# Kernel tuning notes

Hardware: AMD Instinct MI355X
Metric: run time of the kernel (lower is better)

Reference implementation:

```python
import jax, jax.numpy as jnp
import numpy as np

N_NODES = 50000
N_EDGES = 800000
NDIM_IN = 64
EDIM = 64
HID = 152  # size_embedding
NDIM_OUT = 64


def _linear(x, W, b):
    # torch nn.Linear: y = x @ W.T + b
    return jnp.matmul(x, W.T) + b


def _sage_layer(nf, ef, Wm, bm, Wa, ba, src, dst):
    # message: gather src node feats, concat edge feats, linear -> [E,1,F]
    m = _linear(jnp.concatenate([nf[src], ef], axis=2), Wm, bm)
    # mean scatter-reduce to dst nodes (zero for nodes with no in-edges)
    s = jax.ops.segment_sum(m, dst, num_segments=N_NODES)
    deg = jax.ops.segment_sum(jnp.ones((m.shape[0],), m.dtype), dst, num_segments=N_NODES)
    h_neigh = s / jnp.maximum(deg, 1.0)[:, None, None]
    # update: concat self + neighbor agg, linear, relu
    return jax.nn.relu(_linear(jnp.concatenate([nf, h_neigh], axis=2), Wa, ba))


def setup_inputs() -> dict:
    key = jax.random.key(0)
    ks = jax.random.split(key, 16)
    def lin_params(kw, kb, fan_in, fan_out):
        bound = 1.0 / np.sqrt(fan_in)
        W = jax.random.uniform(kw, (fan_out, fan_in), jnp.float32, -bound, bound)
        b = jax.random.uniform(kb, (fan_out,), jnp.float32, -bound, bound)
        return W, b
    nfeats = jax.random.normal(ks[0], (N_NODES, 1, NDIM_IN), jnp.float32)
    efeats = jax.random.normal(ks[1], (N_EDGES, 1, EDIM), jnp.float32)
    src = jax.random.randint(ks[2], (N_EDGES,), 0, N_NODES, jnp.int32)
    dst = jax.random.randint(ks[3], (N_EDGES,), 0, N_NODES, jnp.int32)
    Wm1, bm1 = lin_params(ks[4], ks[5], NDIM_IN + EDIM, HID)
    Wa1, ba1 = lin_params(ks[6], ks[7], NDIM_IN + HID, HID)
    Wm2, bm2 = lin_params(ks[8], ks[9], HID + EDIM, HID)
    Wa2, ba2 = lin_params(ks[10], ks[11], HID + HID, HID)
    Wm3, bm3 = lin_params(ks[12], ks[13], HID + EDIM, NDIM_OUT)
    Wa3, ba3 = lin_params(ks[14], ks[15], HID + NDIM_OUT, NDIM_OUT)
    return {
        "nfeats": nfeats, "efeats": efeats,
        "Wm1": Wm1, "bm1": bm1, "Wa1": Wa1, "ba1": ba1,
        "Wm2": Wm2, "bm2": bm2, "Wa2": Wa2, "ba2": ba2,
        "Wm3": Wm3, "bm3": bm3, "Wa3": Wa3, "ba3": ba3,
        "src": src, "dst": dst,
    }


def reference(nfeats, efeats, Wm1, bm1, Wa1, ba1, Wm2, bm2, Wa2, ba2,
              Wm3, bm3, Wa3, ba3, src, dst):
    # dropout is identity in eval mode
    h = _sage_layer(nfeats, efeats, Wm1, bm1, Wa1, ba1, src, dst)
    h = _sage_layer(h, efeats, Wm2, bm2, Wa2, ba2, src, dst)
    h = _sage_layer(h, efeats, Wm3, bm3, Wa3, ba3, src, dst)
    return h.sum(axis=1)  # [N, ndim_out]
```

## Files before the change

### kernel.cpp

```cpp
#include <hip/hip_runtime.h>


#define NN 50000
#define NE 800000
#define NIN 64
#define EDIM_ 64
#define HID_ 152
#define NOUT 64
#define PADN 50176

__global__ __launch_bounds__(256) void hist_kernel(const int* __restrict__ dst,
                                                   int* __restrict__ ideg) {
    int e = blockIdx.x * 256 + threadIdx.x;
    if (e < NE) atomicAdd(&ideg[dst[e]], 1);
}

__global__ __launch_bounds__(256) void scan1_kernel(const int* __restrict__ in,
                                                    int* __restrict__ out,
                                                    int* __restrict__ bsum) {
    __shared__ int ws[4];
    int t = threadIdx.x;
    int base = blockIdx.x * 1024 + t * 4;
    int a0 = in[base], a1 = in[base + 1], a2 = in[base + 2], a3 = in[base + 3];
    int s = a0 + a1 + a2 + a3;
    int lane = t & 63, wid = t >> 6;
    int v = s;
#pragma unroll
    for (int d = 1; d < 64; d <<= 1) {
        int u = __shfl_up(v, d);
        if (lane >= d) v += u;
    }
    if (lane == 63) ws[wid] = v;
    __syncthreads();
    int wofs = 0;
    if (wid > 0) wofs += ws[0];
    if (wid > 1) wofs += ws[1];
    if (wid > 2) wofs += ws[2];
    int excl = wofs + v - s;
    out[base] = excl;
    out[base + 1] = excl + a0;
    out[base + 2] = excl + a0 + a1;
    out[base + 3] = excl + a0 + a1 + a2;
    if (t == 255) bsum[blockIdx.x] = wofs + v;
}

__global__ __launch_bounds__(64) void scan2_kernel(int* __restrict__ bsum, int nb) {
    int t = threadIdx.x;
    int orig = (t < nb) ? bsum[t] : 0;
    int v = orig;
#pragma unroll
    for (int d = 1; d < 64; d <<= 1) {
        int u = __shfl_up(v, d);
        if (t >= d) v += u;
    }
    if (t < nb) bsum[t] = v - orig;
}

__global__ __launch_bounds__(256) void scan3_kernel(int* __restrict__ out,
                                                    const int* __restrict__ bsum) {
    int base = blockIdx.x * 1024 + threadIdx.x * 4;
    int b = bsum[blockIdx.x];
    out[base] += b; out[base + 1] += b; out[base + 2] += b; out[base + 3] += b;
}

__global__ __launch_bounds__(256) void scatter_edges_kernel(const int* __restrict__ src,
                                                            const int* __restrict__ dst,
                                                            int* __restrict__ cursor,
                                                            int* __restrict__ csr_nf,
                                                            int* __restrict__ csr_ef) {
    int e = blockIdx.x * 256 + threadIdx.x;
    if (e >= NE) return;
    int d = dst[e];
    int pos = atomicAdd(&cursor[d], 1);
    csr_nf[pos] = src[e];
    csr_ef[pos] = e;
}

template <int F>
__global__ __launch_bounds__(256) void agg_kernel(const float* __restrict__ table,
                                                  const int* __restrict__ rows,
                                                  const int* __restrict__ off,
                                                  float* __restrict__ out) {
    constexpr int C = F / 4;
    constexpr int NPW = 64 / C;
    int t = threadIdx.x;
    int lane = t & 63, wid = t >> 6;
    int sub = lane / C;
    int ch = lane - sub * C;
    int n = (blockIdx.x * 4 + wid) * NPW + sub;
    if (sub >= NPW || n >= NN) return;
    int s = off[n], e = off[n + 1];
    float ax0 = 0.f, ax1 = 0.f, ax2 = 0.f, ax3 = 0.f;
    float bx0 = 0.f, bx1 = 0.f, bx2 = 0.f, bx3 = 0.f;
    int i = s;
    for (; i + 1 < e; i += 2) {
        int r0 = rows[i], r1 = rows[i + 1];
        float4 v0 = *(const float4*)(table + (size_t)r0 * F + ch * 4);
        float4 v1 = *(const float4*)(table + (size_t)r1 * F + ch * 4);
        ax0 += v0.x; ax1 += v0.y; ax2 += v0.z; ax3 += v0.w;
        bx0 += v1.x; bx1 += v1.y; bx2 += v1.z; bx3 += v1.w;
    }
    if (i < e) {
        int r0 = rows[i];
        float4 v0 = *(const float4*)(table + (size_t)r0 * F + ch * 4);
        ax0 += v0.x; ax1 += v0.y; ax2 += v0.z; ax3 += v0.w;
    }
    float4 r;
    r.x = ax0 + bx0; r.y = ax1 + bx1; r.z = ax2 + bx2; r.w = ax3 + bx3;
    *(float4*)(out + (size_t)n * F + ch * 4) = r;
}

template <int K1, int K2, int NT, bool MSG>
__global__ __launch_bounds__(256) void gemm_kernel(const float* __restrict__ X1,
                                                   const float* __restrict__ X2,
                                                   const float* __restrict__ W,
                                                   const float* __restrict__ bias,
                                                   const int* __restrict__ off,
                                                   float* __restrict__ out) {
    constexpr int KT = K1 + K2;
    constexpr int NKS = (KT + 15) / 16;
    __shared__ float Xs[16][132];
    __shared__ float Ws[16][68];

    const int t = threadIdx.x;
    const int m0 = blockIdx.x * 128;
    const int n0 = blockIdx.y * 64;

    const int xm = t >> 1;
    const int xh = (t & 1) * 8;
    const int wn = t >> 2;
    const int wc = (t & 3) * 4;

    const int tx = t & 15;
    const int ty = t >> 4;

    const int xrow = m0 + xm;
    const bool xok = xrow < NN;
    const bool wok = (n0 + wn) < NT;
    const float* __restrict__ xrp1 = X1 + (size_t)xrow * K1;
    const float* __restrict__ xrp2 = X2 + (size_t)xrow * K2;
    const float* __restrict__ wrp  = W + (size_t)(n0 + wn) * KT;

    float acc[8][4] = {};
    float4 rx0, rx1, rw;

    auto loadT = [&](int k0) {
        const int kv = k0 + xh;
        rx0 = make_float4(0.f, 0.f, 0.f, 0.f);
        rx1 = rx0;
        if (xok && kv < KT) {
            const float* p = (kv < K1) ? (xrp1 + kv) : (xrp2 + (kv - K1));
            rx0 = *(const float4*)p;
            rx1 = *(const float4*)(p + 4);
        }
        rw = make_float4(0.f, 0.f, 0.f, 0.f);
        const int kw = k0 + wc;
        if (wok && kw < KT) rw = *(const float4*)(wrp + kw);
    };
    auto storeT = [&]() {
        Xs[xh + 0][xm] = rx0.x; Xs[xh + 1][xm] = rx0.y;
        Xs[xh + 2][xm] = rx0.z; Xs[xh + 3][xm] = rx0.w;
        Xs[xh + 4][xm] = rx1.x; Xs[xh + 5][xm] = rx1.y;
        Xs[xh + 6][xm] = rx1.z; Xs[xh + 7][xm] = rx1.w;
        Ws[wc + 0][wn] = rw.x;  Ws[wc + 1][wn] = rw.y;
        Ws[wc + 2][wn] = rw.z;  Ws[wc + 3][wn] = rw.w;
    };

    loadT(0);
    storeT();
    __syncthreads();

    for (int s = 0; s < NKS; ++s) {
        const bool more = (s + 1 < NKS);
        if (more) loadT((s + 1) * 16);
#pragma unroll
        for (int k = 0; k < 16; ++k) {
            const float4 xa = *(const float4*)&Xs[k][ty * 8];
            const float4 xb = *(const float4*)&Xs[k][ty * 8 + 4];
            const float4 wv = *(const float4*)&Ws[k][tx * 4];
            const float xv[8] = {xa.x, xa.y, xa.z, xa.w, xb.x, xb.y, xb.z, xb.w};
#pragma unroll
            for (int i = 0; i < 8; ++i) {
                acc[i][0] += xv[i] * wv.x;
                acc[i][1] += xv[i] * wv.y;
                acc[i][2] += xv[i] * wv.z;
                acc[i][3] += xv[i] * wv.w;
            }
        }
        if (more) {
            __syncthreads();
            storeT();
            __syncthreads();
        }
    }

    const int o0 = n0 + tx * 4;
    if (o0 >= NT) return;
    const float4 bv = *(const float4*)(bias + o0);
#pragma unroll
    for (int i = 0; i < 8; ++i) {
        const int n = m0 + ty * 8 + i;
        if (n >= NN) break;
        float4 r;
        if (MSG) {
            float d = (float)(off[n + 1] - off[n]);
            float inv = 1.0f / fmaxf(d, 1.0f);
            r.x = (acc[i][0] + d * bv.x) * inv;
            r.y = (acc[i][1] + d * bv.y) * inv;
            r.z = (acc[i][2] + d * bv.z) * inv;
            r.w = (acc[i][3] + d * bv.w) * inv;
        } else {
            r.x = fmaxf(acc[i][0] + bv.x, 0.0f);
            r.y = fmaxf(acc[i][1] + bv.y, 0.0f);
            r.z = fmaxf(acc[i][2] + bv.z, 0.0f);
            r.w = fmaxf(acc[i][3] + bv.w, 0.0f);
        }
        *(float4*)(out + (size_t)n * NT + o0) = r;
    }
}

extern "C" void kernel_launch(void* const* d_in, const int* in_sizes, int n_in,
                              void* d_out, int out_size, void* d_ws, size_t ws_size,
                              hipStream_t stream) {
    const float* nfeats = (const float*)d_in[0];
    const float* efeats = (const float*)d_in[1];
    const float* Wm1 = (const float*)d_in[2];
    const float* bm1 = (const float*)d_in[3];
    const float* Wa1 = (const float*)d_in[4];
    const float* ba1 = (const float*)d_in[5];
    const float* Wm2 = (const float*)d_in[6];
    const float* bm2 = (const float*)d_in[7];
    const float* Wa2 = (const float*)d_in[8];
    const float* ba2 = (const float*)d_in[9];
    const float* Wm3 = (const float*)d_in[10];
    const float* bm3 = (const float*)d_in[11];
    const float* Wa3 = (const float*)d_in[12];
    const float* ba3 = (const float*)d_in[13];
    const int* src = (const int*)d_in[14];
    const int* dst = (const int*)d_in[15];
    float* out = (float*)d_out;

    int* iws = (int*)d_ws;
    int* ideg   = iws;
    int* off    = iws + PADN;
    int* cursor = iws + 2 * PADN;
    int* csr_nf = iws + 3 * PADN;
    int* csr_ef = csr_nf + NE;
    float* B = (float*)(csr_ef + NE);
    float* P = B + 3200000;
    float* Q = P + 7600000;
    float* R = Q + 7600000;

    const int BLK = 256;
    auto cdiv = [](long long a, long long b) { return (int)((a + b - 1) / b); };
    dim3 g152(cdiv(NN, 128), cdiv(152, 64));
    dim3 g64(cdiv(NN, 128), 1);
    const int NB = PADN / 1024;

    hipMemsetAsync(ideg, 0, (size_t)PADN * 4, stream);
    hist_kernel<<<cdiv(NE, BLK), BLK, 0, stream>>>(dst, ideg);
    scan1_kernel<<<NB, 256, 0, stream>>>(ideg, off, cursor);
    scan2_kernel<<<1, 64, 0, stream>>>(cursor, NB);
    scan3_kernel<<<NB, 256, 0, stream>>>(off, cursor);
    hipMemcpyAsync(cursor, off, (size_t)NN * 4, hipMemcpyDeviceToDevice, stream);
    scatter_edges_kernel<<<cdiv(NE, BLK), BLK, 0, stream>>>(src, dst, cursor, csr_nf, csr_ef);

    agg_kernel<EDIM_><<<cdiv(NN, 16), BLK, 0, stream>>>(efeats, csr_ef, off, B);

    agg_kernel<NIN><<<cdiv(NN, 16), BLK, 0, stream>>>(nfeats, csr_nf, off, P);
    gemm_kernel<NIN, EDIM_, HID_, true><<<g152, BLK, 0, stream>>>(P, B, Wm1, bm1, off, Q);
    gemm_kernel<NIN, HID_, HID_, false><<<g152, BLK, 0, stream>>>(nfeats, Q, Wa1, ba1, off, R);

    agg_kernel<HID_><<<cdiv(NN, 4), BLK, 0, stream>>>(R, csr_nf, off, P);
    gemm_kernel<HID_, EDIM_, HID_, true><<<g152, BLK, 0, stream>>>(P, B, Wm2, bm2, off, Q);
    gemm_kernel<HID_, HID_, HID_, false><<<g152, BLK, 0, stream>>>(R, Q, Wa2, ba2, off, P);

    agg_kernel<HID_><<<cdiv(NN, 4), BLK, 0, stream>>>(P, csr_nf, off, Q);
    gemm_kernel<HID_, EDIM_, NOUT, true><<<g64, BLK, 0, stream>>>(Q, B, Wm3, bm3, off, R);
    gemm_kernel<HID_, NOUT, NOUT, false><<<g64, BLK, 0, stream>>>(P, R, Wa3, ba3, off, out);
}
```

Baseline: 1.001 ms.

## Replace FP32 SIMT GEMMs with split-FP16 MFMA GEMMs

Rewrites the six dense GEMMs to use 16x16x32 FP16 MFMA instructions. FP32 accuracy is kept by splitting each operand into hi and lo halves and issuing three MFMAs per tile. Weights are split ahead of time by a new per-call kernel into padded hi/lo FP16 buffers, while activations are split while being staged to shared memory. The aim is to move the GEMM work off scalar FMA onto matrix cores. The costs are extra conversion work, six small extra launches, and scalar epilogue stores instead of float4 stores.

```diff
diff --git a/kernel.cpp b/kernel.cpp
--- a/kernel.cpp
+++ b/kernel.cpp
@@ -8,6 +8,10 @@
 #define HID_ 152
 #define NOUT 64
 #define PADN 50176
+
+typedef float f4v __attribute__((ext_vector_type(4)));
+typedef _Float16 h8v __attribute__((ext_vector_type(8)));
+typedef _Float16 h4v __attribute__((ext_vector_type(4)));
 
 __global__ __launch_bounds__(256) void hist_kernel(const int* __restrict__ dst,
                                                    int* __restrict__ ideg) {
@@ -110,61 +114,94 @@
     *(float4*)(out + (size_t)n * F + ch * 4) = r;
 }
 
-template <int K1, int K2, int NT, bool MSG>
-__global__ __launch_bounds__(256) void gemm_kernel(const float* __restrict__ X1,
-                                                   const float* __restrict__ X2,
-                                                   const float* __restrict__ W,
-                                                   const float* __restrict__ bias,
-                                                   const int* __restrict__ off,
-                                                   float* __restrict__ out) {
-    constexpr int KT = K1 + K2;
-    constexpr int NKS = (KT + 15) / 16;
-    __shared__ float Xs[16][132];
-    __shared__ float Ws[16][68];
+__global__ __launch_bounds__(256) void wsplit_kernel(const float* __restrict__ W,
+                                                     _Float16* __restrict__ hi,
+                                                     _Float16* __restrict__ lo,
+                                                     int NT, int Kin1, int K1P,
+                                                     int Kin2, int KTP, int total) {
+    int e = blockIdx.x * 256 + threadIdx.x;
+    if (e >= total) return;
+    int n = e / KTP, k = e - n * KTP;
+    float v = 0.f;
+    if (n < NT) {
+        int s = -1;
+        if (k < K1P) { if (k < Kin1) s = k; }
+        else { int k2 = k - K1P; if (k2 < Kin2) s = Kin1 + k2; }
+        if (s >= 0) v = W[(size_t)n * (Kin1 + Kin2) + s];
+    }
+    _Float16 h = (_Float16)v;
+    hi[e] = h;
+    lo[e] = (_Float16)(v - (float)h);
+}
+
+template <int K1P, int K2P, int K1, int K2, int NT, bool MSG>
+__global__ __launch_bounds__(256) void mgemm_kernel(const float* __restrict__ X1,
+                                                    const float* __restrict__ X2,
+                                                    const _Float16* __restrict__ Whi,
+                                                    const _Float16* __restrict__ Wlo,
+                                                    const float* __restrict__ bias,
+                                                    const int* __restrict__ off,
+                                                    float* __restrict__ out) {
+    constexpr int KTP = K1P + K2P;
+    constexpr int NKS = KTP / 32;
+    __shared__ _Float16 sm[12288];
 
     const int t = threadIdx.x;
     const int m0 = blockIdx.x * 128;
     const int n0 = blockIdx.y * 64;
 
-    const int xm = t >> 1;
-    const int xh = (t & 1) * 8;
-    const int wn = t >> 2;
-    const int wc = (t & 3) * 4;
-
-    const int tx = t & 15;
-    const int ty = t >> 4;
-
-    const int xrow = m0 + xm;
-    const bool xok = xrow < NN;
-    const bool wok = (n0 + wn) < NT;
-    const float* __restrict__ xrp1 = X1 + (size_t)xrow * K1;
-    const float* __restrict__ xrp2 = X2 + (size_t)xrow * K2;
-    const float* __restrict__ wrp  = W + (size_t)(n0 + wn) * KT;
-
-    float acc[8][4] = {};
-    float4 rx0, rx1, rw;
+    const int ar = t >> 3;
+    const int akc = (t & 7) * 4;
+    const int br = t >> 2;
+    const int bkc = (t & 3) * 8;
+    const _Float16* wph = Whi + (size_t)(n0 + br) * KTP + bkc;
+    const _Float16* wpl = Wlo + (size_t)(n0 + br) * KTP + bkc;
+
+    f4v ax[4];
+    h8v bxh, bxl;
 
     auto loadT = [&](int k0) {
-        const int kv = k0 + xh;
-        rx0 = make_float4(0.f, 0.f, 0.f, 0.f);
-        rx1 = rx0;
-        if (xok && kv < KT) {
-            const float* p = (kv < K1) ? (xrp1 + kv) : (xrp2 + (kv - K1));
-            rx0 = *(const float4*)p;
-            rx1 = *(const float4*)(p + 4);
-        }
-        rw = make_float4(0.f, 0.f, 0.f, 0.f);
-        const int kw = k0 + wc;
-        if (wok && kw < KT) rw = *(const float4*)(wrp + kw);
+        const float* Xp; int Ka, kb;
+        if (k0 < K1P) { Xp = X1; Ka = K1; kb = k0; }
+        else          { Xp = X2; Ka = K2; kb = k0 - K1P; }
+        const int kg = kb + akc;
+        const bool kok = kg < Ka;
+        f4v z = {0.f, 0.f, 0.f, 0.f};
+#pragma unroll
+        for (int i = 0; i < 4; ++i) {
+            const int row = m0 + ar + 32 * i;
+            ax[i] = (kok && row < NN) ? *(const f4v*)(Xp + (size_t)row * Ka + kg) : z;
+        }
+        bxh = *(const h8v*)(wph + k0);
+        bxl = *(const h8v*)(wpl + k0);
     };
     auto storeT = [&]() {
-        Xs[xh + 0][xm] = rx0.x; Xs[xh + 1][xm] = rx0.y;
-        Xs[xh + 2][xm] = rx0.z; Xs[xh + 3][xm] = rx0.w;
-        Xs[xh + 4][xm] = rx1.x; Xs[xh + 5][xm] = rx1.y;
-        Xs[xh + 6][xm] = rx1.z; Xs[xh + 7][xm] = rx1.w;
-        Ws[wc + 0][wn] = rw.x;  Ws[wc + 1][wn] = rw.y;
-        Ws[wc + 2][wn] = rw.z;  Ws[wc + 3][wn] = rw.w;
+#pragma unroll
+        for (int i = 0; i < 4; ++i) {
+            h4v hi, lo;
+#pragma unroll
+            for (int j = 0; j < 4; ++j) {
+                float v = ax[i][j];
+                _Float16 h = (_Float16)v;
+                hi[j] = h;
+                lo[j] = (_Float16)(v - (float)h);
+            }
+            const int d = (ar + 32 * i) * 32 + akc;
+            *(h4v*)(sm + d) = hi;
+            *(h4v*)(sm + 4096 + d) = lo;
+        }
+        const int bd = br * 32 + bkc;
+        *(h8v*)(sm + 8192 + bd) = bxh;
+        *(h8v*)(sm + 10240 + bd) = bxl;
     };
+
+    const int lane = t & 63, wid = t >> 6;
+    const int wm = wid >> 1, wn = wid & 1;
+    const int lr = lane & 15, g = lane >> 4;
+    const int aoff = (wm * 64 + lr) * 32 + g * 8;
+    const int boff = (wn * 32 + lr) * 32 + g * 8;
+
+    f4v acc[4][2] = {};
 
     loadT(0);
     storeT();
@@ -172,21 +209,26 @@
 
     for (int s = 0; s < NKS; ++s) {
         const bool more = (s + 1 < NKS);
-        if (more) loadT((s + 1) * 16);
-#pragma unroll
-        for (int k = 0; k < 16; ++k) {
-            const float4 xa = *(const float4*)&Xs[k][ty * 8];
-            const float4 xb = *(const float4*)&Xs[k][ty * 8 + 4];
-            const float4 wv = *(const float4*)&Ws[k][tx * 4];
-            const float xv[8] = {xa.x, xa.y, xa.z, xa.w, xb.x, xb.y, xb.z, xb.w};
-#pragma unroll
-            for (int i = 0; i < 8; ++i) {
-                acc[i][0] += xv[i] * wv.x;
-                acc[i][1] += xv[i] * wv.y;
-                acc[i][2] += xv[i] * wv.z;
-                acc[i][3] += xv[i] * wv.w;
+        if (more) loadT((s + 1) * 32);
+        h8v ah[4], al[4], bh[2], bl[2];
+#pragma unroll
+        for (int mf = 0; mf < 4; ++mf) {
+            ah[mf] = *(const h8v*)(sm + aoff + mf * 512);
+            al[mf] = *(const h8v*)(sm + 4096 + aoff + mf * 512);
+        }
+#pragma unroll
+        for (int nf = 0; nf < 2; ++nf) {
+            bh[nf] = *(const h8v*)(sm + 8192 + boff + nf * 512);
+            bl[nf] = *(const h8v*)(sm + 10240 + boff + nf * 512);
+        }
+#pragma unroll
+        for (int mf = 0; mf < 4; ++mf)
+#pragma unroll
+            for (int nf = 0; nf < 2; ++nf) {
+                acc[mf][nf] = __builtin_amdgcn_mfma_f32_16x16x32_f16(ah[mf], bh[nf], acc[mf][nf], 0, 0, 0);
+                acc[mf][nf] = __builtin_amdgcn_mfma_f32_16x16x32_f16(ah[mf], bl[nf], acc[mf][nf], 0, 0, 0);
+                acc[mf][nf] = __builtin_amdgcn_mfma_f32_16x16x32_f16(al[mf], bh[nf], acc[mf][nf], 0, 0, 0);
             }
-        }
         if (more) {
             __syncthreads();
             storeT();
@@ -194,28 +236,27 @@
         }
     }
 
-    const int o0 = n0 + tx * 4;
-    if (o0 >= NT) return;
-    const float4 bv = *(const float4*)(bias + o0);
-#pragma unroll
-    for (int i = 0; i < 8; ++i) {
-        const int n = m0 + ty * 8 + i;
-        if (n >= NN) break;
-        float4 r;
-        if (MSG) {
-            float d = (float)(off[n + 1] - off[n]);
-            float inv = 1.0f / fmaxf(d, 1.0f);
-            r.x = (acc[i][0] + d * bv.x) * inv;
-            r.y = (acc[i][1] + d * bv.y) * inv;
-            r.z = (acc[i][2] + d * bv.z) * inv;
-            r.w = (acc[i][3] + d * bv.w) * inv;
-        } else {
-            r.x = fmaxf(acc[i][0] + bv.x, 0.0f);
-            r.y = fmaxf(acc[i][1] + bv.y, 0.0f);
-            r.z = fmaxf(acc[i][2] + bv.z, 0.0f);
-            r.w = fmaxf(acc[i][3] + bv.w, 0.0f);
-        }
-        *(float4*)(out + (size_t)n * NT + o0) = r;
+#pragma unroll
+    for (int mf = 0; mf < 4; ++mf) {
+#pragma unroll
+        for (int r = 0; r < 4; ++r) {
+            const int m = m0 + wm * 64 + mf * 16 + g * 4 + r;
+            if (m >= NN) continue;
+            float dv = 0.f, inv = 0.f;
+            if (MSG) {
+                dv = (float)(off[m + 1] - off[m]);
+                inv = 1.0f / fmaxf(dv, 1.0f);
+            }
+#pragma unroll
+            for (int nf = 0; nf < 2; ++nf) {
+                const int n = n0 + wn * 32 + nf * 16 + lr;
+                if (n >= NT) continue;
+                const float a = acc[mf][nf][r];
+                const float val = MSG ? (a + dv * bias[n]) * inv
+                                      : fmaxf(a + bias[n], 0.0f);
+                out[(size_t)m * NT + n] = val;
+            }
+        }
     }
 }
 
@@ -250,12 +291,31 @@
     float* P = B + 3200000;
     float* Q = P + 7600000;
     float* R = Q + 7600000;
+    _Float16* w1h = (_Float16*)(R + 7600000);
+    _Float16* w1l = w1h + 24576;
+    _Float16* w2h = w1l + 24576;
+    _Float16* w2l = w2h + 43008;
+    _Float16* w3h = w2l + 43008;
+    _Float16* w3l = w3h + 43008;
+    _Float16* w4h = w3l + 43008;
+    _Float16* w4l = w4h + 61440;
+    _Float16* w5h = w4l + 61440;
+    _Float16* w5l = w5h + 14336;
+    _Float16* w6h = w5l + 14336;
+    _Float16* w6l = w6h + 14336;
 
     const int BLK = 256;
     auto cdiv = [](long long a, long long b) { return (int)((a + b - 1) / b); };
-    dim3 g152(cdiv(NN, 128), cdiv(152, 64));
+    dim3 g152(cdiv(NN, 128), 3);
     dim3 g64(cdiv(NN, 128), 1);
     const int NB = PADN / 1024;
+
+    wsplit_kernel<<<96,  BLK, 0, stream>>>(Wm1, w1h, w1l, 152, 64, 64, 64, 128, 24576);
+    wsplit_kernel<<<168, BLK, 0, stream>>>(Wa1, w2h, w2l, 152, 64, 64, 152, 224, 43008);
+    wsplit_kernel<<<168, BLK, 0, stream>>>(Wm2, w3h, w3l, 152, 152, 160, 64, 224, 43008);
+    wsplit_kernel<<<240, BLK, 0, stream>>>(Wa2, w4h, w4l, 152, 152, 160, 152, 320, 61440);
+    wsplit_kernel<<<56,  BLK, 0, stream>>>(Wm3, w5h, w5l, 64, 152, 160, 64, 224, 14336);
+    wsplit_kernel<<<56,  BLK, 0, stream>>>(Wa3, w6h, w6l, 64, 152, 160, 64, 224, 14336);
 
     hipMemsetAsync(ideg, 0, (size_t)PADN * 4, stream);
     hist_kernel<<<cdiv(NE, BLK), BLK, 0, stream>>>(dst, ideg);
@@ -268,14 +328,14 @@
     agg_kernel<EDIM_><<<cdiv(NN, 16), BLK, 0, stream>>>(efeats, csr_ef, off, B);
 
     agg_kernel<NIN><<<cdiv(NN, 16), BLK, 0, stream>>>(nfeats, csr_nf, off, P);
-    gemm_kernel<NIN, EDIM_, HID_, true><<<g152, BLK, 0, stream>>>(P, B, Wm1, bm1, off, Q);
-    gemm_kernel<NIN, HID_, HID_, false><<<g152, BLK, 0, stream>>>(nfeats, Q, Wa1, ba1, off, R);
+    mgemm_kernel<64, 64, 64, 64, HID_, true><<<g152, BLK, 0, stream>>>(P, B, w1h, w1l, bm1, off, Q);
+    mgemm_kernel<64, 160, 64, 152, HID_, false><<<g152, BLK, 0, stream>>>(nfeats, Q, w2h, w2l, ba1, off, R);
 
     agg_kernel<HID_><<<cdiv(NN, 4), BLK, 0, stream>>>(R, csr_nf, off, P);
-    gemm_kernel<HID_, EDIM_, HID_, true><<<g152, BLK, 0, stream>>>(P, B, Wm2, bm2, off, Q);
-    gemm_kernel<HID_, HID_, HID_, false><<<g152, BLK, 0, stream>>>(R, Q, Wa2, ba2, off, P);
+    mgemm_kernel<160, 64, 152, 64, HID_, true><<<g152, BLK, 0, stream>>>(P, B, w3h, w3l, bm2, off, Q);
+    mgemm_kernel<160, 160, 152, 152, HID_, false><<<g152, BLK, 0, stream>>>(R, Q, w4h, w4l, ba2, off, P);
 
     agg_kernel<HID_><<<cdiv(NN, 4), BLK, 0, stream>>>(P, csr_nf, off, Q);
-    gemm_kernel<HID_, EDIM_, NOUT, true><<<g64, BLK, 0, stream>>>(Q, B, Wm3, bm3, off, R);
-    gemm_kernel<HID_, NOUT, NOUT, false><<<g64, BLK, 0, stream>>>(P, R, Wa3, ba3, off, out);
-}
+    mgemm_kernel<160, 64, 152, 64, NOUT, true><<<g64, BLK, 0, stream>>>(Q, B, w5h, w5l, bm3, off, R);
+    mgemm_kernel<160, 64, 152, 64, NOUT, false><<<g64, BLK, 0, stream>>>(P, R, w6h, w6l, ba3, off, out);
+}
```

Result: faster. 824.6 us (-17.6%).
